# Performance work log

Measured on AMD Instinct MI355X. Metric: run time of the kernel, lower is better.

## Reference

```python
import jax, jax.numpy as jnp
import numpy as np

NUM_CLASSES = 1000
FEAT_DIM = 256
BATCH = 8192
MARGIN = 5.0
ALPHA = 1.0
BETA = 1.0


def setup_inputs() -> dict:
    key = jax.random.key(0)
    k1, k2, k3 = jax.random.split(key, 3)
    x = jax.random.normal(k1, (BATCH, FEAT_DIM), dtype=jnp.float32)
    labels = jax.random.randint(k2, (BATCH,), 0, NUM_CLASSES, dtype=jnp.int64)
    centers = jax.random.normal(k3, (NUM_CLASSES, FEAT_DIM), dtype=jnp.float32)
    return {"x": x, "labels": labels, "centers": centers}


def reference(x, labels, centers):
    # --- intra-class part ---
    # distmat_intra[i, j] = ||x_i||^2 + ||x_j||^2 - 2 x_i . x_j  (then relu + sqrt)
    mag = jnp.sum(x * x, axis=1)                      # (B,)
    sim = x @ x.T                                     # (B, B)
    d2 = mag[None, :] + mag[:, None] - 2.0 * sim      # (B, B)
    d = jnp.sqrt(jax.nn.relu(d2))                     # (B, B)

    # mask[i, j] = labels[i] == labels[j]; original gathers masked values per row,
    # clamps to [1e-12, 1e12], sorts descending and uses only the top-2 values.
    mask = labels[:, None] == labels[None, :]         # (B, B) bool
    vals = jnp.where(mask, jnp.clip(d, 1e-12, 1e12), -jnp.inf)
    top2, _ = jax.lax.top_k(vals.reshape(-1), 2)      # two largest intra-class dists
    k = 2.0
    loss_intra = k / (1.0 / top2[0] + 1.0 / top2[1])  # harmonic mean * k

    # --- inter-class part (faithful to original broadcasting) ---
    # distmat_inter[i, j] = 2 ||c_j||^2 - 2 c_i . c_j
    cmag = 2.0 * jnp.sum(centers * centers, axis=1)   # (C,)
    inter = cmag[None, :] - 2.0 * (centers @ centers.T)
    inter = jnp.clip(inter.reshape(-1), 1e-12, 1e12)
    loss_inter = jnp.clip(MARGIN - jnp.min(inter), 0.0, 1e6)

    return ALPHA * loss_intra + BETA * loss_inter
```

## Files before the change

kernel.cpp:

```cpp
#include <hip/hip_runtime.h>
#include <math.h>

#define BATCH 8192
#define FEAT  256
#define NCLS  1000

#define REPL    2
#define NINTRA  (REPL*NCLS)
#define NGEMM   528
#define NBLK    (NINTRA + NGEMM)
#define ROWCAP  16
#define MEMCAP  96


__global__ __launch_bounds__(256) void k_main(const float* __restrict__ x,
                                              const int* __restrict__ labels,
                                              const float* __restrict__ centers,
                                              float* __restrict__ ws) {
    __shared__ __align__(16) char raw[17152];
    __shared__ float wred[4];
    __shared__ int cnt;
    int t = threadIdx.x;
    int lane = t & 63, w = t >> 6;

    if (blockIdx.x < NINTRA) {
        int bid = blockIdx.x;
        int c   = bid >> 1;
        int r   = bid & 1;
        float (*rowS)[256] = reinterpret_cast<float(*)[256]>(raw);
        int*   mem  = reinterpret_cast<int*>(raw + 16384);
        float* magS = reinterpret_cast<float*>(raw + 16768);

        if (t == 0) cnt = 0;
        __syncthreads();
        const int4* gl4 = reinterpret_cast<const int4*>(labels);
        #pragma unroll
        for (int k = 0; k < 8; ++k) {
            int4 lv = gl4[t + (k << 8)];
            int base = (t + (k << 8)) << 2;
            if (lv.x == c) { int p = atomicAdd(&cnt, 1); if (p < MEMCAP) mem[p] = base;     }
            if (lv.y == c) { int p = atomicAdd(&cnt, 1); if (p < MEMCAP) mem[p] = base + 1; }
            if (lv.z == c) { int p = atomicAdd(&cnt, 1); if (p < MEMCAP) mem[p] = base + 2; }
            if (lv.w == c) { int p = atomicAdd(&cnt, 1); if (p < MEMCAP) mem[p] = base + 3; }
        }
        __syncthreads();
        int n = cnt < MEMCAP ? cnt : MEMCAP;
        float vmax = 0.0f;
        if (n >= 2) {
            const float4* x4 = reinterpret_cast<const float4*>(x);
            for (int m = w; m < n; m += 4) {
                int row = mem[m];
                float4 v = x4[(size_t)row * 64 + lane];
                if (m < ROWCAP)
                    *reinterpret_cast<float4*>(&rowS[m][lane << 2]) = v;
                float s = v.x * v.x + v.y * v.y + v.z * v.z + v.w * v.w;
                #pragma unroll
                for (int o = 32; o > 0; o >>= 1) s += __shfl_xor(s, o);
                if (lane == 0) magS[m] = s;
            }
            __syncthreads();
            int npairs = n * (n - 1) / 2;
            for (int p = r * 4 + w; p < npairs; p += 8) {
                int a = 0, rem = p;
                while (rem >= n - 1 - a) { rem -= n - 1 - a; ++a; }
                int b = a + 1 + rem;
                float4 va = (a < ROWCAP)
                    ? *reinterpret_cast<float4*>(&rowS[a][lane << 2])
                    : x4[(size_t)mem[a] * 64 + lane];
                float4 vb = (b < ROWCAP)
                    ? *reinterpret_cast<float4*>(&rowS[b][lane << 2])
                    : x4[(size_t)mem[b] * 64 + lane];
                float s = va.x * vb.x + va.y * vb.y + va.z * vb.z + va.w * vb.w;
                #pragma unroll
                for (int o = 32; o > 0; o >>= 1) s += __shfl_xor(s, o);
                float d2 = magS[a] + magS[b] - 2.0f * s;
                float d  = sqrtf(fmaxf(d2, 0.0f));
                d = fminf(fmaxf(d, 1e-12f), 1e12f);
                vmax = fmaxf(vmax, d);
            }
        }
        if (lane == 0) wred[w] = vmax;
        __syncthreads();
        if (t == 0) {
            float m = fmaxf(fmaxf(wred[0], wred[1]), fmaxf(wred[2], wred[3]));
            ws[bid] = m;
        }
    } else {
        float (*As)[34] = reinterpret_cast<float(*)[34]>(raw);
        float (*Bs)[34] = reinterpret_cast<float(*)[34]>(raw + 4352);
        float* cmagI    = reinterpret_cast<float*>(raw + 8704);
        float* cmagJ    = reinterpret_cast<float*>(raw + 8832);

        int bi = 0, rem = blockIdx.x - NINTRA;
        while (rem >= 32 - bi) { rem -= 32 - bi; ++bi; }
        int bj = bi + rem;
        int i0 = bi * 32, j0 = bj * 32;

        for (int q = w; q < 32; q += 4) {
            int gi = i0 + q, gj = j0 + q;
            float sI = 0.0f, sJ = 0.0f;
            if (gi < NCLS) {
                float4 v = reinterpret_cast<const float4*>(centers + (size_t)gi * FEAT)[lane];
                sI = v.x * v.x + v.y * v.y + v.z * v.z + v.w * v.w;
            }
            if (gj < NCLS) {
                float4 v = reinterpret_cast<const float4*>(centers + (size_t)gj * FEAT)[lane];
                sJ = v.x * v.x + v.y * v.y + v.z * v.z + v.w * v.w;
            }
            #pragma unroll
            for (int o = 32; o > 0; o >>= 1) {
                sI += __shfl_xor(sI, o);
                sJ += __shfl_xor(sJ, o);
            }
            if (lane == 0) { cmagI[q] = 2.0f * sI; cmagJ[q] = 2.0f * sJ; }
        }

        int tx = t & 15, ty = t >> 4;
        float acc[2][2] = {{0.f, 0.f}, {0.f, 0.f}};
        for (int kk = 0; kk < FEAT; kk += 32) {
            {
                int row = t >> 3, q = t & 7;
                int col = kk + q * 4;
                int gi = i0 + row, gj = j0 + row;
                float4 av = (gi < NCLS)
                    ? *reinterpret_cast<const float4*>(centers + (size_t)gi * FEAT + col)
                    : make_float4(0.f, 0.f, 0.f, 0.f);
                float4 bv = (gj < NCLS)
                    ? *reinterpret_cast<const float4*>(centers + (size_t)gj * FEAT + col)
                    : make_float4(0.f, 0.f, 0.f, 0.f);
                As[q * 4 + 0][row] = av.x; As[q * 4 + 1][row] = av.y;
                As[q * 4 + 2][row] = av.z; As[q * 4 + 3][row] = av.w;
                Bs[q * 4 + 0][row] = bv.x; Bs[q * 4 + 1][row] = bv.y;
                Bs[q * 4 + 2][row] = bv.z; Bs[q * 4 + 3][row] = bv.w;
            }
            __syncthreads();
            #pragma unroll
            for (int k = 0; k < 32; ++k) {
                float2 a2 = *reinterpret_cast<float2*>(&As[k][ty * 2]);
                float2 b2 = *reinterpret_cast<float2*>(&Bs[k][tx * 2]);
                acc[0][0] += a2.x * b2.x; acc[0][1] += a2.x * b2.y;
                acc[1][0] += a2.y * b2.x; acc[1][1] += a2.y * b2.y;
            }
            __syncthreads();
        }
        float lmin = 1e30f;
        #pragma unroll
        for (int jj = 0; jj < 2; ++jj) {
            int J = j0 + tx * 2 + jj;
            #pragma unroll
            for (int ii = 0; ii < 2; ++ii) {
                int I = i0 + ty * 2 + ii;
                if (I < NCLS && J < NCLS) {
                    float v1 = cmagJ[tx * 2 + jj] - 2.0f * acc[ii][jj];
                    v1 = fminf(fmaxf(v1, 1e-12f), 1e12f);
                    float v2 = cmagI[ty * 2 + ii] - 2.0f * acc[ii][jj];
                    v2 = fminf(fmaxf(v2, 1e-12f), 1e12f);
                    lmin = fminf(lmin, fminf(v1, v2));
                }
            }
        }
        #pragma unroll
        for (int o = 32; o > 0; o >>= 1) lmin = fminf(lmin, __shfl_xor(lmin, o));
        if (lane == 0) wred[w] = lmin;
        __syncthreads();
        if (t == 0) {
            float m = fminf(fminf(wred[0], wred[1]), fminf(wred[2], wred[3]));
            ws[blockIdx.x] = m;
        }
    }
}

__global__ __launch_bounds__(256) void k_final(const float* __restrict__ ws,
                                               float* __restrict__ out) {
    __shared__ float smx[4], smn[4];
    int t = threadIdx.x, lane = t & 63, w = t >> 6;
    float mn = 1e30f, mx = 0.0f;
    for (int i = t; i < NINTRA; i += 256) mx = fmaxf(mx, ws[i]);
    for (int i = t; i < NGEMM; i += 256)  mn = fminf(mn, ws[NINTRA + i]);
    #pragma unroll
    for (int o = 32; o > 0; o >>= 1) {
        mx = fmaxf(mx, __shfl_xor(mx, o));
        mn = fminf(mn, __shfl_xor(mn, o));
    }
    if (lane == 0) { smx[w] = mx; smn[w] = mn; }
    __syncthreads();
    if (t == 0) {
        mx = fmaxf(fmaxf(smx[0], smx[1]), fmaxf(smx[2], smx[3]));
        mn = fminf(fminf(smn[0], smn[1]), fminf(smn[2], smn[3]));
        float M = fmaxf(mx, 1e-12f);
        float r = 1.0f / M;
        float li2 = 2.0f / (r + r);
        float m = fminf(mn, 1e12f);
        float linter = fminf(fmaxf(5.0f - m, 0.0f), 1e6f);
        out[0] = li2 + linter;
    }
}

extern "C" void kernel_launch(void* const* d_in, const int* in_sizes, int n_in,
                              void* d_out, int out_size, void* d_ws, size_t ws_size,
                              hipStream_t stream) {
    const float* x       = (const float*)d_in[0];
    const int*   labels  = (const int*)d_in[1];
    const float* centers = (const float*)d_in[2];
    float*        ws     = (float*)d_ws;
    float*        out    = (float*)d_out;

    k_main<<<NBLK, 256, 0, stream>>>(x, labels, centers, ws);
    k_final<<<1, 256, 0, stream>>>(ws, out);
}
```

Baseline: 101.7 us.

## Schedule GEMM blocks first and unroll intra-class row loading by two

Reorders the fused grid so the 528 center-GEMM blocks get the low block indices and are dispatched before the intra-class blocks. The replica index now comes from the upper half of the range instead of the low bit, so replicas of one class are no longer adjacent. The row-loading loop in the intra blocks now issues two global row loads per wave per iteration to expose more memory parallelism. The aim is to keep the heavier GEMM blocks off the tail and shorten load latency, at the cost of slightly more register use and changed ordering in the workspace reduction.

New measurement: 94.77 us. -6.9%, faster.

```diff
diff --git a/kernel.cpp b/kernel.cpp
--- a/kernel.cpp
+++ b/kernel.cpp
@@ -5,10 +5,10 @@
 #define FEAT  256
 #define NCLS  1000
 
+#define NGEMM   528
 #define REPL    2
 #define NINTRA  (REPL*NCLS)
-#define NGEMM   528
-#define NBLK    (NINTRA + NGEMM)
+#define NBLK    (NGEMM + NINTRA)
 #define ROWCAP  16
 #define MEMCAP  96
 
@@ -23,10 +23,92 @@
     int t = threadIdx.x;
     int lane = t & 63, w = t >> 6;
 
-    if (blockIdx.x < NINTRA) {
-        int bid = blockIdx.x;
-        int c   = bid >> 1;
-        int r   = bid & 1;
+    if (blockIdx.x < NGEMM) {
+        float (*As)[34] = reinterpret_cast<float(*)[34]>(raw);
+        float (*Bs)[34] = reinterpret_cast<float(*)[34]>(raw + 4352);
+        float* cmagI    = reinterpret_cast<float*>(raw + 8704);
+        float* cmagJ    = reinterpret_cast<float*>(raw + 8832);
+
+        int bi = 0, rem = blockIdx.x;
+        while (rem >= 32 - bi) { rem -= 32 - bi; ++bi; }
+        int bj = bi + rem;
+        int i0 = bi * 32, j0 = bj * 32;
+
+        for (int q = w; q < 32; q += 4) {
+            int gi = i0 + q, gj = j0 + q;
+            float sI = 0.0f, sJ = 0.0f;
+            if (gi < NCLS) {
+                float4 v = reinterpret_cast<const float4*>(centers + (size_t)gi * FEAT)[lane];
+                sI = v.x * v.x + v.y * v.y + v.z * v.z + v.w * v.w;
+            }
+            if (gj < NCLS) {
+                float4 v = reinterpret_cast<const float4*>(centers + (size_t)gj * FEAT)[lane];
+                sJ = v.x * v.x + v.y * v.y + v.z * v.z + v.w * v.w;
+            }
+            #pragma unroll
+            for (int o = 32; o > 0; o >>= 1) {
+                sI += __shfl_xor(sI, o);
+                sJ += __shfl_xor(sJ, o);
+            }
+            if (lane == 0) { cmagI[q] = 2.0f * sI; cmagJ[q] = 2.0f * sJ; }
+        }
+
+        int tx = t & 15, ty = t >> 4;
+        float acc[2][2] = {{0.f, 0.f}, {0.f, 0.f}};
+        for (int kk = 0; kk < FEAT; kk += 32) {
+            {
+                int row = t >> 3, q = t & 7;
+                int col = kk + q * 4;
+                int gi = i0 + row, gj = j0 + row;
+                float4 av = (gi < NCLS)
+                    ? *reinterpret_cast<const float4*>(centers + (size_t)gi * FEAT + col)
+                    : make_float4(0.f, 0.f, 0.f, 0.f);
+                float4 bv = (gj < NCLS)
+                    ? *reinterpret_cast<const float4*>(centers + (size_t)gj * FEAT + col)
+                    : make_float4(0.f, 0.f, 0.f, 0.f);
+                As[q * 4 + 0][row] = av.x; As[q * 4 + 1][row] = av.y;
+                As[q * 4 + 2][row] = av.z; As[q * 4 + 3][row] = av.w;
+                Bs[q * 4 + 0][row] = bv.x; Bs[q * 4 + 1][row] = bv.y;
+                Bs[q * 4 + 2][row] = bv.z; Bs[q * 4 + 3][row] = bv.w;
+            }
+            __syncthreads();
+            #pragma unroll
+            for (int k = 0; k < 32; ++k) {
+                float2 a2 = *reinterpret_cast<float2*>(&As[k][ty * 2]);
+                float2 b2 = *reinterpret_cast<float2*>(&Bs[k][tx * 2]);
+                acc[0][0] += a2.x * b2.x; acc[0][1] += a2.x * b2.y;
+                acc[1][0] += a2.y * b2.x; acc[1][1] += a2.y * b2.y;
+            }
+            __syncthreads();
+        }
+        float lmin = 1e30f;
+        #pragma unroll
+        for (int jj = 0; jj < 2; ++jj) {
+            int J = j0 + tx * 2 + jj;
+            #pragma unroll
+            for (int ii = 0; ii < 2; ++ii) {
+                int I = i0 + ty * 2 + ii;
+                if (I < NCLS && J < NCLS) {
+                    float v1 = cmagJ[tx * 2 + jj] - 2.0f * acc[ii][jj];
+                    v1 = fminf(fmaxf(v1, 1e-12f), 1e12f);
+                    float v2 = cmagI[ty * 2 + ii] - 2.0f * acc[ii][jj];
+                    v2 = fminf(fmaxf(v2, 1e-12f), 1e12f);
+                    lmin = fminf(lmin, fminf(v1, v2));
+                }
+            }
+        }
+        #pragma unroll
+        for (int o = 32; o > 0; o >>= 1) lmin = fminf(lmin, __shfl_xor(lmin, o));
+        if (lane == 0) wred[w] = lmin;
+        __syncthreads();
+        if (t == 0) {
+            float m = fminf(fminf(wred[0], wred[1]), fminf(wred[2], wred[3]));
+            ws[blockIdx.x] = m;
+        }
+    } else {
+        int bid = blockIdx.x - NGEMM;
+        int c   = (bid < NCLS) ? bid : bid - NCLS;
+        int r   = (bid < NCLS) ? 0 : 1;
         float (*rowS)[256] = reinterpret_cast<float(*)[256]>(raw);
         int*   mem  = reinterpret_cast<int*>(raw + 16384);
         float* magS = reinterpret_cast<float*>(raw + 16768);
@@ -48,15 +130,27 @@
         float vmax = 0.0f;
         if (n >= 2) {
             const float4* x4 = reinterpret_cast<const float4*>(x);
-            for (int m = w; m < n; m += 4) {
-                int row = mem[m];
-                float4 v = x4[(size_t)row * 64 + lane];
+            for (int m = w; m < n; m += 8) {
+                int m2 = m + 4;
+                bool has2 = (m2 < n);
+                float4 v0 = x4[(size_t)mem[m] * 64 + lane];
+                float4 v1 = has2 ? x4[(size_t)mem[m2] * 64 + lane]
+                                 : make_float4(0.f, 0.f, 0.f, 0.f);
                 if (m < ROWCAP)
-                    *reinterpret_cast<float4*>(&rowS[m][lane << 2]) = v;
-                float s = v.x * v.x + v.y * v.y + v.z * v.z + v.w * v.w;
+                    *reinterpret_cast<float4*>(&rowS[m][lane << 2]) = v0;
+                if (has2 && m2 < ROWCAP)
+                    *reinterpret_cast<float4*>(&rowS[m2][lane << 2]) = v1;
+                float s0 = v0.x * v0.x + v0.y * v0.y + v0.z * v0.z + v0.w * v0.w;
+                float s1 = v1.x * v1.x + v1.y * v1.y + v1.z * v1.z + v1.w * v1.w;
                 #pragma unroll
-                for (int o = 32; o > 0; o >>= 1) s += __shfl_xor(s, o);
-                if (lane == 0) magS[m] = s;
+                for (int o = 32; o > 0; o >>= 1) {
+                    s0 += __shfl_xor(s0, o);
+                    s1 += __shfl_xor(s1, o);
+                }
+                if (lane == 0) {
+                    magS[m] = s0;
+                    if (has2) magS[m2] = s1;
+                }
             }
             __syncthreads();
             int npairs = n * (n - 1) / 2;
@@ -83,88 +177,6 @@
         __syncthreads();
         if (t == 0) {
             float m = fmaxf(fmaxf(wred[0], wred[1]), fmaxf(wred[2], wred[3]));
-            ws[bid] = m;
-        }
-    } else {
-        float (*As)[34] = reinterpret_cast<float(*)[34]>(raw);
-        float (*Bs)[34] = reinterpret_cast<float(*)[34]>(raw + 4352);
-        float* cmagI    = reinterpret_cast<float*>(raw + 8704);
-        float* cmagJ    = reinterpret_cast<float*>(raw + 8832);
-
-        int bi = 0, rem = blockIdx.x - NINTRA;
-        while (rem >= 32 - bi) { rem -= 32 - bi; ++bi; }
-        int bj = bi + rem;
-        int i0 = bi * 32, j0 = bj * 32;
-
-        for (int q = w; q < 32; q += 4) {
-            int gi = i0 + q, gj = j0 + q;
-            float sI = 0.0f, sJ = 0.0f;
-            if (gi < NCLS) {
-                float4 v = reinterpret_cast<const float4*>(centers + (size_t)gi * FEAT)[lane];
-                sI = v.x * v.x + v.y * v.y + v.z * v.z + v.w * v.w;
-            }
-            if (gj < NCLS) {
-                float4 v = reinterpret_cast<const float4*>(centers + (size_t)gj * FEAT)[lane];
-                sJ = v.x * v.x + v.y * v.y + v.z * v.z + v.w * v.w;
-            }
-            #pragma unroll
-            for (int o = 32; o > 0; o >>= 1) {
-                sI += __shfl_xor(sI, o);
-                sJ += __shfl_xor(sJ, o);
-            }
-            if (lane == 0) { cmagI[q] = 2.0f * sI; cmagJ[q] = 2.0f * sJ; }
-        }
-
-        int tx = t & 15, ty = t >> 4;
-        float acc[2][2] = {{0.f, 0.f}, {0.f, 0.f}};
-        for (int kk = 0; kk < FEAT; kk += 32) {
-            {
-                int row = t >> 3, q = t & 7;
-                int col = kk + q * 4;
-                int gi = i0 + row, gj = j0 + row;
-                float4 av = (gi < NCLS)
-                    ? *reinterpret_cast<const float4*>(centers + (size_t)gi * FEAT + col)
-                    : make_float4(0.f, 0.f, 0.f, 0.f);
-                float4 bv = (gj < NCLS)
-                    ? *reinterpret_cast<const float4*>(centers + (size_t)gj * FEAT + col)
-                    : make_float4(0.f, 0.f, 0.f, 0.f);
-                As[q * 4 + 0][row] = av.x; As[q * 4 + 1][row] = av.y;
-                As[q * 4 + 2][row] = av.z; As[q * 4 + 3][row] = av.w;
-                Bs[q * 4 + 0][row] = bv.x; Bs[q * 4 + 1][row] = bv.y;
-                Bs[q * 4 + 2][row] = bv.z; Bs[q * 4 + 3][row] = bv.w;
-            }
-            __syncthreads();
-            #pragma unroll
-            for (int k = 0; k < 32; ++k) {
-                float2 a2 = *reinterpret_cast<float2*>(&As[k][ty * 2]);
-                float2 b2 = *reinterpret_cast<float2*>(&Bs[k][tx * 2]);
-                acc[0][0] += a2.x * b2.x; acc[0][1] += a2.x * b2.y;
-                acc[1][0] += a2.y * b2.x; acc[1][1] += a2.y * b2.y;
-            }
-            __syncthreads();
-        }
-        float lmin = 1e30f;
-        #pragma unroll
-        for (int jj = 0; jj < 2; ++jj) {
-            int J = j0 + tx * 2 + jj;
-            #pragma unroll
-            for (int ii = 0; ii < 2; ++ii) {
-                int I = i0 + ty * 2 + ii;
-                if (I < NCLS && J < NCLS) {
-                    float v1 = cmagJ[tx * 2 + jj] - 2.0f * acc[ii][jj];
-                    v1 = fminf(fmaxf(v1, 1e-12f), 1e12f);
-                    float v2 = cmagI[ty * 2 + ii] - 2.0f * acc[ii][jj];
-                    v2 = fminf(fmaxf(v2, 1e-12f), 1e12f);
-                    lmin = fminf(lmin, fminf(v1, v2));
-                }
-            }
-        }
-        #pragma unroll
-        for (int o = 32; o > 0; o >>= 1) lmin = fminf(lmin, __shfl_xor(lmin, o));
-        if (lane == 0) wred[w] = lmin;
-        __syncthreads();
-        if (t == 0) {
-            float m = fminf(fminf(wred[0], wred[1]), fminf(wred[2], wred[3]));
             ws[blockIdx.x] = m;
         }
     }
@@ -175,8 +187,8 @@
     __shared__ float smx[4], smn[4];
     int t = threadIdx.x, lane = t & 63, w = t >> 6;
     float mn = 1e30f, mx = 0.0f;
-    for (int i = t; i < NINTRA; i += 256) mx = fmaxf(mx, ws[i]);
-    for (int i = t; i < NGEMM; i += 256)  mn = fminf(mn, ws[NINTRA + i]);
+    for (int i = t; i < NGEMM; i += 256)  mn = fminf(mn, ws[i]);
+    for (int i = t; i < NINTRA; i += 256) mx = fmaxf(mx, ws[NGEMM + i]);
     #pragma unroll
     for (int o = 32; o > 0; o >>= 1) {
         mx = fmaxf(mx, __shfl_xor(mx, o));
```

## Split fused kernel into separate intra and inter kernels with 512-thread intra blocks

Applied to the files above, without the earlier changes.

Replaces the single fused kernel (two replica blocks per class plus GEMM blocks) with a dedicated intra-class kernel using one 512-thread block per class and a separate inter-class GEMM kernel. The intra kernel processes two pairs per wave per iteration for more ILP and caches up to 24 rows in shared memory instead of 16. This halves the number of label scans but adds a kernel launch and serialises the intra and inter stages on the stream instead of running them concurrently.

Measured after the change: 100.4 us. Within noise of the previous version (-1.3%).

```diff
diff --git a/kernel.cpp b/kernel.cpp
--- a/kernel.cpp
+++ b/kernel.cpp
@@ -5,168 +5,186 @@
 #define FEAT  256
 #define NCLS  1000
 
-#define REPL    2
-#define NINTRA  (REPL*NCLS)
 #define NGEMM   528
-#define NBLK    (NINTRA + NGEMM)
-#define ROWCAP  16
+#define NINTRA  NCLS
+#define ROWCAP  24
 #define MEMCAP  96
 
 
-__global__ __launch_bounds__(256) void k_main(const float* __restrict__ x,
-                                              const int* __restrict__ labels,
-                                              const float* __restrict__ centers,
-                                              float* __restrict__ ws) {
-    __shared__ __align__(16) char raw[17152];
-    __shared__ float wred[4];
+__global__ __launch_bounds__(512) void k_intra(const float* __restrict__ x,
+                                               const int* __restrict__ labels,
+                                               float* __restrict__ ws) {
+    __shared__ __align__(16) float rowS[ROWCAP][256];
+    __shared__ int   mem[MEMCAP];
+    __shared__ float magS[MEMCAP];
+    __shared__ float wred[8];
     __shared__ int cnt;
     int t = threadIdx.x;
     int lane = t & 63, w = t >> 6;
-
-    if (blockIdx.x < NINTRA) {
-        int bid = blockIdx.x;
-        int c   = bid >> 1;
-        int r   = bid & 1;
-        float (*rowS)[256] = reinterpret_cast<float(*)[256]>(raw);
-        int*   mem  = reinterpret_cast<int*>(raw + 16384);
-        float* magS = reinterpret_cast<float*>(raw + 16768);
-
-        if (t == 0) cnt = 0;
+    int c = blockIdx.x;
+
+    if (t == 0) cnt = 0;
+    __syncthreads();
+    const int4* gl4 = reinterpret_cast<const int4*>(labels);
+    #pragma unroll
+    for (int k = 0; k < 4; ++k) {
+        int idx = t + (k << 9);
+        int4 lv = gl4[idx];
+        int base = idx << 2;
+        if (lv.x == c) { int p = atomicAdd(&cnt, 1); if (p < MEMCAP) mem[p] = base;     }
+        if (lv.y == c) { int p = atomicAdd(&cnt, 1); if (p < MEMCAP) mem[p] = base + 1; }
+        if (lv.z == c) { int p = atomicAdd(&cnt, 1); if (p < MEMCAP) mem[p] = base + 2; }
+        if (lv.w == c) { int p = atomicAdd(&cnt, 1); if (p < MEMCAP) mem[p] = base + 3; }
+    }
+    __syncthreads();
+    int n = cnt < MEMCAP ? cnt : MEMCAP;
+    float vmax = 0.0f;
+    if (n >= 2) {
+        const float4* x4 = reinterpret_cast<const float4*>(x);
+        for (int m = w; m < n; m += 8) {
+            float4 v = x4[(size_t)mem[m] * 64 + lane];
+            if (m < ROWCAP)
+                *reinterpret_cast<float4*>(&rowS[m][lane << 2]) = v;
+            float s = v.x * v.x + v.y * v.y + v.z * v.z + v.w * v.w;
+            #pragma unroll
+            for (int o = 32; o > 0; o >>= 1) s += __shfl_xor(s, o);
+            if (lane == 0) magS[m] = s;
+        }
         __syncthreads();
-        const int4* gl4 = reinterpret_cast<const int4*>(labels);
-        #pragma unroll
-        for (int k = 0; k < 8; ++k) {
-            int4 lv = gl4[t + (k << 8)];
-            int base = (t + (k << 8)) << 2;
-            if (lv.x == c) { int p = atomicAdd(&cnt, 1); if (p < MEMCAP) mem[p] = base;     }
-            if (lv.y == c) { int p = atomicAdd(&cnt, 1); if (p < MEMCAP) mem[p] = base + 1; }
-            if (lv.z == c) { int p = atomicAdd(&cnt, 1); if (p < MEMCAP) mem[p] = base + 2; }
-            if (lv.w == c) { int p = atomicAdd(&cnt, 1); if (p < MEMCAP) mem[p] = base + 3; }
-        }
-        __syncthreads();
-        int n = cnt < MEMCAP ? cnt : MEMCAP;
-        float vmax = 0.0f;
-        if (n >= 2) {
-            const float4* x4 = reinterpret_cast<const float4*>(x);
-            for (int m = w; m < n; m += 4) {
-                int row = mem[m];
-                float4 v = x4[(size_t)row * 64 + lane];
-                if (m < ROWCAP)
-                    *reinterpret_cast<float4*>(&rowS[m][lane << 2]) = v;
-                float s = v.x * v.x + v.y * v.y + v.z * v.z + v.w * v.w;
-                #pragma unroll
-                for (int o = 32; o > 0; o >>= 1) s += __shfl_xor(s, o);
-                if (lane == 0) magS[m] = s;
-            }
-            __syncthreads();
-            int npairs = n * (n - 1) / 2;
-            for (int p = r * 4 + w; p < npairs; p += 8) {
-                int a = 0, rem = p;
-                while (rem >= n - 1 - a) { rem -= n - 1 - a; ++a; }
-                int b = a + 1 + rem;
-                float4 va = (a < ROWCAP)
-                    ? *reinterpret_cast<float4*>(&rowS[a][lane << 2])
-                    : x4[(size_t)mem[a] * 64 + lane];
-                float4 vb = (b < ROWCAP)
-                    ? *reinterpret_cast<float4*>(&rowS[b][lane << 2])
-                    : x4[(size_t)mem[b] * 64 + lane];
-                float s = va.x * vb.x + va.y * vb.y + va.z * vb.z + va.w * vb.w;
-                #pragma unroll
-                for (int o = 32; o > 0; o >>= 1) s += __shfl_xor(s, o);
-                float d2 = magS[a] + magS[b] - 2.0f * s;
-                float d  = sqrtf(fmaxf(d2, 0.0f));
-                d = fminf(fmaxf(d, 1e-12f), 1e12f);
-                vmax = fmaxf(vmax, d);
-            }
-        }
-        if (lane == 0) wred[w] = vmax;
-        __syncthreads();
-        if (t == 0) {
-            float m = fmaxf(fmaxf(wred[0], wred[1]), fmaxf(wred[2], wred[3]));
-            ws[bid] = m;
-        }
-    } else {
-        float (*As)[34] = reinterpret_cast<float(*)[34]>(raw);
-        float (*Bs)[34] = reinterpret_cast<float(*)[34]>(raw + 4352);
-        float* cmagI    = reinterpret_cast<float*>(raw + 8704);
-        float* cmagJ    = reinterpret_cast<float*>(raw + 8832);
-
-        int bi = 0, rem = blockIdx.x - NINTRA;
-        while (rem >= 32 - bi) { rem -= 32 - bi; ++bi; }
-        int bj = bi + rem;
-        int i0 = bi * 32, j0 = bj * 32;
-
-        for (int q = w; q < 32; q += 4) {
-            int gi = i0 + q, gj = j0 + q;
-            float sI = 0.0f, sJ = 0.0f;
-            if (gi < NCLS) {
-                float4 v = reinterpret_cast<const float4*>(centers + (size_t)gi * FEAT)[lane];
-                sI = v.x * v.x + v.y * v.y + v.z * v.z + v.w * v.w;
-            }
-            if (gj < NCLS) {
-                float4 v = reinterpret_cast<const float4*>(centers + (size_t)gj * FEAT)[lane];
-                sJ = v.x * v.x + v.y * v.y + v.z * v.z + v.w * v.w;
-            }
+        int npairs = n * (n - 1) / 2;
+        for (int p = w; p < npairs; p += 16) {
+            int p2 = p + 8;
+            bool has2 = (p2 < npairs);
+            int a1 = 0, r1 = p;
+            while (r1 >= n - 1 - a1) { r1 -= n - 1 - a1; ++a1; }
+            int b1 = a1 + 1 + r1;
+            int a2 = a1, b2 = b1;
+            if (has2) {
+                int r2 = p2; a2 = 0;
+                while (r2 >= n - 1 - a2) { r2 -= n - 1 - a2; ++a2; }
+                b2 = a2 + 1 + r2;
+            }
+            float4 va1 = (a1 < ROWCAP) ? *reinterpret_cast<float4*>(&rowS[a1][lane << 2])
+                                       : x4[(size_t)mem[a1] * 64 + lane];
+            float4 vb1 = (b1 < ROWCAP) ? *reinterpret_cast<float4*>(&rowS[b1][lane << 2])
+                                       : x4[(size_t)mem[b1] * 64 + lane];
+            float4 va2 = (a2 < ROWCAP) ? *reinterpret_cast<float4*>(&rowS[a2][lane << 2])
+                                       : x4[(size_t)mem[a2] * 64 + lane];
+            float4 vb2 = (b2 < ROWCAP) ? *reinterpret_cast<float4*>(&rowS[b2][lane << 2])
+                                       : x4[(size_t)mem[b2] * 64 + lane];
+            float s1 = va1.x * vb1.x + va1.y * vb1.y + va1.z * vb1.z + va1.w * vb1.w;
+            float s2 = va2.x * vb2.x + va2.y * vb2.y + va2.z * vb2.z + va2.w * vb2.w;
             #pragma unroll
             for (int o = 32; o > 0; o >>= 1) {
-                sI += __shfl_xor(sI, o);
-                sJ += __shfl_xor(sJ, o);
-            }
-            if (lane == 0) { cmagI[q] = 2.0f * sI; cmagJ[q] = 2.0f * sJ; }
-        }
-
-        int tx = t & 15, ty = t >> 4;
-        float acc[2][2] = {{0.f, 0.f}, {0.f, 0.f}};
-        for (int kk = 0; kk < FEAT; kk += 32) {
-            {
-                int row = t >> 3, q = t & 7;
-                int col = kk + q * 4;
-                int gi = i0 + row, gj = j0 + row;
-                float4 av = (gi < NCLS)
-                    ? *reinterpret_cast<const float4*>(centers + (size_t)gi * FEAT + col)
-                    : make_float4(0.f, 0.f, 0.f, 0.f);
-                float4 bv = (gj < NCLS)
-                    ? *reinterpret_cast<const float4*>(centers + (size_t)gj * FEAT + col)
-                    : make_float4(0.f, 0.f, 0.f, 0.f);
-                As[q * 4 + 0][row] = av.x; As[q * 4 + 1][row] = av.y;
-                As[q * 4 + 2][row] = av.z; As[q * 4 + 3][row] = av.w;
-                Bs[q * 4 + 0][row] = bv.x; Bs[q * 4 + 1][row] = bv.y;
-                Bs[q * 4 + 2][row] = bv.z; Bs[q * 4 + 3][row] = bv.w;
-            }
-            __syncthreads();
-            #pragma unroll
-            for (int k = 0; k < 32; ++k) {
-                float2 a2 = *reinterpret_cast<float2*>(&As[k][ty * 2]);
-                float2 b2 = *reinterpret_cast<float2*>(&Bs[k][tx * 2]);
-                acc[0][0] += a2.x * b2.x; acc[0][1] += a2.x * b2.y;
-                acc[1][0] += a2.y * b2.x; acc[1][1] += a2.y * b2.y;
-            }
-            __syncthreads();
-        }
-        float lmin = 1e30f;
-        #pragma unroll
-        for (int jj = 0; jj < 2; ++jj) {
-            int J = j0 + tx * 2 + jj;
-            #pragma unroll
-            for (int ii = 0; ii < 2; ++ii) {
-                int I = i0 + ty * 2 + ii;
-                if (I < NCLS && J < NCLS) {
-                    float v1 = cmagJ[tx * 2 + jj] - 2.0f * acc[ii][jj];
-                    v1 = fminf(fmaxf(v1, 1e-12f), 1e12f);
-                    float v2 = cmagI[ty * 2 + ii] - 2.0f * acc[ii][jj];
-                    v2 = fminf(fmaxf(v2, 1e-12f), 1e12f);
-                    lmin = fminf(lmin, fminf(v1, v2));
-                }
-            }
-        }
-        #pragma unroll
-        for (int o = 32; o > 0; o >>= 1) lmin = fminf(lmin, __shfl_xor(lmin, o));
-        if (lane == 0) wred[w] = lmin;
+                s1 += __shfl_xor(s1, o);
+                s2 += __shfl_xor(s2, o);
+            }
+            float d2a = magS[a1] + magS[b1] - 2.0f * s1;
+            float da  = sqrtf(fmaxf(d2a, 0.0f));
+            da = fminf(fmaxf(da, 1e-12f), 1e12f);
+            vmax = fmaxf(vmax, da);
+            if (has2) {
+                float d2b = magS[a2] + magS[b2] - 2.0f * s2;
+                float db  = sqrtf(fmaxf(d2b, 0.0f));
+                db = fminf(fmaxf(db, 1e-12f), 1e12f);
+                vmax = fmaxf(vmax, db);
+            }
+        }
+    }
+    if (lane == 0) wred[w] = vmax;
+    __syncthreads();
+    if (t == 0) {
+        float m = 0.0f;
+        #pragma unroll
+        for (int q = 0; q < 8; ++q) m = fmaxf(m, wred[q]);
+        ws[NGEMM + c] = m;
+    }
+}
+
+__global__ __launch_bounds__(256) void k_inter(const float* __restrict__ centers,
+                                               float* __restrict__ ws) {
+    __shared__ float As[32][34];
+    __shared__ float Bs[32][34];
+    __shared__ float cmagI[32], cmagJ[32];
+    __shared__ float wred[4];
+    int t = threadIdx.x;
+    int lane = t & 63, w = t >> 6;
+
+    int bi = 0, rem = blockIdx.x;
+    while (rem >= 32 - bi) { rem -= 32 - bi; ++bi; }
+    int bj = bi + rem;
+    int i0 = bi * 32, j0 = bj * 32;
+
+    for (int q = w; q < 32; q += 4) {
+        int gi = i0 + q, gj = j0 + q;
+        float sI = 0.0f, sJ = 0.0f;
+        if (gi < NCLS) {
+            float4 v = reinterpret_cast<const float4*>(centers + (size_t)gi * FEAT)[lane];
+            sI = v.x * v.x + v.y * v.y + v.z * v.z + v.w * v.w;
+        }
+        if (gj < NCLS) {
+            float4 v = reinterpret_cast<const float4*>(centers + (size_t)gj * FEAT)[lane];
+            sJ = v.x * v.x + v.y * v.y + v.z * v.z + v.w * v.w;
+        }
+        #pragma unroll
+        for (int o = 32; o > 0; o >>= 1) {
+            sI += __shfl_xor(sI, o);
+            sJ += __shfl_xor(sJ, o);
+        }
+        if (lane == 0) { cmagI[q] = 2.0f * sI; cmagJ[q] = 2.0f * sJ; }
+    }
+
+    int tx = t & 15, ty = t >> 4;
+    float acc[2][2] = {{0.f, 0.f}, {0.f, 0.f}};
+    for (int kk = 0; kk < FEAT; kk += 32) {
+        {
+            int row = t >> 3, q = t & 7;
+            int col = kk + q * 4;
+            int gi = i0 + row, gj = j0 + row;
+            float4 av = (gi < NCLS)
+                ? *reinterpret_cast<const float4*>(centers + (size_t)gi * FEAT + col)
+                : make_float4(0.f, 0.f, 0.f, 0.f);
+            float4 bv = (gj < NCLS)
+                ? *reinterpret_cast<const float4*>(centers + (size_t)gj * FEAT + col)
+                : make_float4(0.f, 0.f, 0.f, 0.f);
+            As[q * 4 + 0][row] = av.x; As[q * 4 + 1][row] = av.y;
+            As[q * 4 + 2][row] = av.z; As[q * 4 + 3][row] = av.w;
+            Bs[q * 4 + 0][row] = bv.x; Bs[q * 4 + 1][row] = bv.y;
+            Bs[q * 4 + 2][row] = bv.z; Bs[q * 4 + 3][row] = bv.w;
+        }
         __syncthreads();
-        if (t == 0) {
-            float m = fminf(fminf(wred[0], wred[1]), fminf(wred[2], wred[3]));
-            ws[blockIdx.x] = m;
-        }
+        #pragma unroll
+        for (int k = 0; k < 32; ++k) {
+            float2 a2 = *reinterpret_cast<float2*>(&As[k][ty * 2]);
+            float2 b2 = *reinterpret_cast<float2*>(&Bs[k][tx * 2]);
+            acc[0][0] += a2.x * b2.x; acc[0][1] += a2.x * b2.y;
+            acc[1][0] += a2.y * b2.x; acc[1][1] += a2.y * b2.y;
+        }
+        __syncthreads();
+    }
+    float lmin = 1e30f;
+    #pragma unroll
+    for (int jj = 0; jj < 2; ++jj) {
+        int J = j0 + tx * 2 + jj;
+        #pragma unroll
+        for (int ii = 0; ii < 2; ++ii) {
+            int I = i0 + ty * 2 + ii;
+            if (I < NCLS && J < NCLS) {
+                float v1 = cmagJ[tx * 2 + jj] - 2.0f * acc[ii][jj];
+                v1 = fminf(fmaxf(v1, 1e-12f), 1e12f);
+                float v2 = cmagI[ty * 2 + ii] - 2.0f * acc[ii][jj];
+                v2 = fminf(fmaxf(v2, 1e-12f), 1e12f);
+                lmin = fminf(lmin, fminf(v1, v2));
+            }
+        }
+    }
+    #pragma unroll
+    for (int o = 32; o > 0; o >>= 1) lmin = fminf(lmin, __shfl_xor(lmin, o));
+    if (lane == 0) wred[w] = lmin;
+    __syncthreads();
+    if (t == 0) {
+        float m = fminf(fminf(wred[0], wred[1]), fminf(wred[2], wred[3]));
+        ws[blockIdx.x] = m;
     }
 }
 
@@ -175,8 +193,8 @@
     __shared__ float smx[4], smn[4];
     int t = threadIdx.x, lane = t & 63, w = t >> 6;
     float mn = 1e30f, mx = 0.0f;
-    for (int i = t; i < NINTRA; i += 256) mx = fmaxf(mx, ws[i]);
-    for (int i = t; i < NGEMM; i += 256)  mn = fminf(mn, ws[NINTRA + i]);
+    for (int i = t; i < NGEMM; i += 256)  mn = fminf(mn, ws[i]);
+    for (int i = t; i < NINTRA; i += 256) mx = fmaxf(mx, ws[NGEMM + i]);
     #pragma unroll
     for (int o = 32; o > 0; o >>= 1) {
         mx = fmaxf(mx, __shfl_xor(mx, o));
@@ -205,6 +223,7 @@
     float*        ws     = (float*)d_ws;
     float*        out    = (float*)d_out;
 
-    k_main<<<NBLK, 256, 0, stream>>>(x, labels, centers, ws);
+    k_intra<<<NINTRA, 512, 0, stream>>>(x, labels, ws);
+    k_inter<<<NGEMM, 256, 0, stream>>>(centers, ws);
     k_final<<<1, 256, 0, stream>>>(ws, out);
 }
```
